# Performance work log

Hardware: AMD Instinct MI355X
Metric: run time of the kernel (lower is better)

## Reference

```python
import jax, jax.numpy as jnp
import numpy as np
from jax import lax

T, B, N_IN, H, N_OUT = 2048, 64, 128, 256, 128

def setup_inputs() -> dict:
    key = jax.random.key(0)
    ks = jax.random.split(key, 7)
    s_ih = 1.0 / np.sqrt(H)
    return {
        "x": jax.random.normal(ks[0], (T, B, N_IN), jnp.float32),
        "w_ih": jax.random.uniform(ks[1], (H, N_IN), jnp.float32, -s_ih, s_ih),
        "w_hh": jax.random.uniform(ks[2], (H, H), jnp.float32, -s_ih, s_ih),
        "b_ih": jax.random.uniform(ks[3], (H,), jnp.float32, -s_ih, s_ih),
        "b_hh": jax.random.uniform(ks[4], (H,), jnp.float32, -s_ih, s_ih),
        "w_out": jax.random.uniform(ks[5], (N_OUT, H), jnp.float32, -1.0/np.sqrt(H), 1.0/np.sqrt(H)),
        "b_out": jax.random.uniform(ks[6], (N_OUT,), jnp.float32, -1.0/np.sqrt(H), 1.0/np.sqrt(H)),
    }

def reference(x, w_ih, w_hh, b_ih, b_hh, w_out, b_out):
    # Vanilla RNN (basic_rnn_step): h_t = tanh(x_t W_ih^T + b_ih + h_{t-1} W_hh^T + b_hh)
    # Precompute input projections for all timesteps in one big GEMM.
    x_proj = jnp.einsum('tbi,hi->tbh', x, w_ih) + b_ih + b_hh  # [T,B,H]

    def step(h, xp_t):
        h = jnp.tanh(xp_t + h @ w_hh.T)
        return h, h

    h0 = jnp.zeros((x.shape[1], w_hh.shape[0]), x.dtype)
    _, hs = lax.scan(step, h0, x_proj)          # hs: [T,B,H]
    # Linear output layer applied at every timestep (has_fc_out -> logits)
    return jnp.einsum('tbh,oh->tbo', hs, w_out) + b_out
```

## Files before the change

### kernel.cpp

```cpp
#include <hip/hip_runtime.h>
#include <hip/hip_bf16.h>
#include <hip/hip_fp16.h>

#define T_ 2048
#define B_ 64
#define NIN_ 128
#define H_ 256
#define NOUT_ 128
#define TB_ (T_*B_)
#define BH_ (B_*H_)
#define TBLK2_ (T_/16)

typedef _Float16 h8 __attribute__((ext_vector_type(8)));
typedef float f32x4 __attribute__((ext_vector_type(4)));

#define BAR_LGKM() asm volatile("s_waitcnt lgkmcnt(0)\n\ts_barrier" ::: "memory")

__device__ __forceinline__ h8 cvt8(float4 a, float4 b) {
    h8 r;
    r[0] = (_Float16)a.x; r[1] = (_Float16)a.y; r[2] = (_Float16)a.z; r[3] = (_Float16)a.w;
    r[4] = (_Float16)b.x; r[5] = (_Float16)b.y; r[6] = (_Float16)b.z; r[7] = (_Float16)b.w;
    return r;
}
__device__ __forceinline__ h8 ld_cvt8(const float* __restrict__ p) {
    const float4* q = (const float4*)p;
    return cvt8(q[0], q[1]);
}

__global__ __launch_bounds__(768, 1) void k2_scan(
    const float* __restrict__ x,
    const float* __restrict__ w_ih,
    const float* __restrict__ w_hh,
    const float* __restrict__ b_ih,
    const float* __restrict__ b_hh,
    _Float16* __restrict__ hs)
{
    const int tid = threadIdx.x;
    const int lane = tid & 63, wave = tid >> 6;
    const int n = lane & 15, quad = lane >> 4;
    const int b = blockIdx.x;

    __shared__ __align__(16) _Float16 hb[2][256];
    __shared__ __align__(16) _Float16 xpb[2][256][24];

    if (wave < 8) {
        const int tsel = quad & 1;
        const int j = wave*32 + tsel*16 + n;
        const bool writer = (quad < 2);

        h8 bf[2][8];
        #pragma unroll
        for (int t = 0; t < 2; ++t)
            #pragma unroll
            for (int kt = 0; kt < 8; ++kt)
                bf[t][kt] = ld_cvt8(w_hh + (size_t)(wave*32 + t*16 + n) * H_ + kt*32 + quad*8);

        if (tid < 256) hb[0][tid] = (_Float16)0.0f;
        asm volatile("s_waitcnt lgkmcnt(0) vmcnt(0)" ::: "memory");
        __builtin_amdgcn_s_barrier();

        _Float16* hsl = hs + (size_t)b * H_ + j;

#define K2_STEP(T, RB, WB, XV)                                                 \
    {                                                                          \
        const h8* hp = (const h8*)&RB[0];                                      \
        h8 av[8];                                                              \
        _Pragma("unroll")                                                      \
        for (int kt = 0; kt < 8; ++kt) av[kt] = hp[kt*4 + quad];               \
        f32x4 acc[2];                                                          \
        acc[0] = (f32x4){0,0,0,0}; acc[1] = (f32x4){0,0,0,0};                  \
        __builtin_amdgcn_s_setprio(1);                                         \
        _Pragma("unroll")                                                      \
        for (int kt = 0; kt < 8; ++kt) {                                       \
            acc[0] = __builtin_amdgcn_mfma_f32_16x16x32_f16(av[kt], bf[0][kt], acc[0], 0, 0, 0); \
            acc[1] = __builtin_amdgcn_mfma_f32_16x16x32_f16(av[kt], bf[1][kt], acc[1], 0, 0, 0); \
        }                                                                      \
        __builtin_amdgcn_s_setprio(0);                                         \
        float vv = tsel ? acc[1][0] : acc[0][0];                               \
        float sv = vv + (XV);                                                  \
        float e  = __expf(2.0f * sv);                                          \
        float hn = fmaf(-2.0f, __builtin_amdgcn_rcpf(e + 1.0f), 1.0f);         \
        _Float16 h16 = (_Float16)hn;                                           \
        if (writer) {                                                          \
            WB[j] = h16;                                                       \
            hsl[(size_t)(T) * BH_] = h16;                                      \
        }                                                                      \
        BAR_LGKM();                                                            \
    }

        for (int tb = 0; tb < TBLK2_; ++tb) {
            const int p = tb & 1;
            const int t0 = tb * 16;
            h8 cur0 = *(const h8*)&xpb[p][j][0];
            K2_STEP(t0 + 0, hb[0], hb[1], (float)cur0[0])
            K2_STEP(t0 + 1, hb[1], hb[0], (float)cur0[1])
            K2_STEP(t0 + 2, hb[0], hb[1], (float)cur0[2])
            K2_STEP(t0 + 3, hb[1], hb[0], (float)cur0[3])
            K2_STEP(t0 + 4, hb[0], hb[1], (float)cur0[4])
            K2_STEP(t0 + 5, hb[1], hb[0], (float)cur0[5])
            K2_STEP(t0 + 6, hb[0], hb[1], (float)cur0[6])
            K2_STEP(t0 + 7, hb[1], hb[0], (float)cur0[7])
            h8 cur1 = *(const h8*)&xpb[p][j][8];
            K2_STEP(t0 + 8,  hb[0], hb[1], (float)cur1[0])
            K2_STEP(t0 + 9,  hb[1], hb[0], (float)cur1[1])
            K2_STEP(t0 + 10, hb[0], hb[1], (float)cur1[2])
            K2_STEP(t0 + 11, hb[1], hb[0], (float)cur1[3])
            K2_STEP(t0 + 12, hb[0], hb[1], (float)cur1[4])
            K2_STEP(t0 + 13, hb[1], hb[0], (float)cur1[5])
            K2_STEP(t0 + 14, hb[0], hb[1], (float)cur1[6])
            K2_STEP(t0 + 15, hb[1], hb[0], (float)cur1[7])
        }
#undef K2_STEP
    } else {
        const int w = wave - 8;
        const int m = n;

        h8 aih[4][4];
        #pragma unroll
        for (int i = 0; i < 4; ++i)
            #pragma unroll
            for (int kt = 0; kt < 4; ++kt)
                aih[i][kt] = ld_cvt8(w_ih + (size_t)(w*64 + i*16 + m) * NIN_ + kt*32 + quad*8);

        float xb2[4][4];
        #pragma unroll
        for (int i = 0; i < 4; ++i)
            #pragma unroll
            for (int r = 0; r < 4; ++r) {
                int c = w*64 + i*16 + quad*4 + r;
                xb2[i][r] = b_ih[c] + b_hh[c];
            }

        float4 xr[4][2];
        h8 bx[4];
        f32x4 xacc[4];

#define LOAD_X(blk)                                                            \
    {                                                                          \
        _Pragma("unroll")                                                      \
        for (int kt = 0; kt < 4; ++kt) {                                       \
            const float4* q = (const float4*)(x + ((size_t)((blk)*16 + m) * B_ + b) * NIN_ + kt*32 + quad*8); \
            xr[kt][0] = q[0]; xr[kt][1] = q[1];                                \
        }                                                                      \
    }

#define XPROJ_PIECE(kt)                                                        \
    {                                                                          \
        _Pragma("unroll")                                                      \
        for (int i = 0; i < 4; ++i)                                            \
            xacc[i] = __builtin_amdgcn_mfma_f32_16x16x32_f16(aih[i][kt], bx[kt], xacc[i], 0, 0, 0); \
    }

#define XPROJ_WRITE(buf)                                                       \
    {                                                                          \
        _Pragma("unroll")                                                      \
        for (int i = 0; i < 4; ++i)                                            \
            _Pragma("unroll")                                                  \
            for (int r = 0; r < 4; ++r) {                                      \
                int c = w*64 + i*16 + quad*4 + r;                              \
                xpb[buf][c][m] = (_Float16)(xacc[i][r] + xb2[i][r]);           \
            }                                                                  \
    }

        LOAD_X(0);
        #pragma unroll
        for (int kt = 0; kt < 4; ++kt) bx[kt] = cvt8(xr[kt][0], xr[kt][1]);
        #pragma unroll
        for (int i = 0; i < 4; ++i) xacc[i] = (f32x4){0,0,0,0};
        #pragma unroll
        for (int kt = 0; kt < 4; ++kt) XPROJ_PIECE(kt)
        XPROJ_WRITE(0);
        LOAD_X(1);
        asm volatile("s_waitcnt lgkmcnt(0) vmcnt(0)" ::: "memory");
        __builtin_amdgcn_s_barrier();

        for (int tb = 0; tb < TBLK2_; ++tb) {
            const int p = tb & 1;
            const bool gen = (tb < TBLK2_ - 1);
            if (gen) {
                #pragma unroll
                for (int kt = 0; kt < 4; ++kt) bx[kt] = cvt8(xr[kt][0], xr[kt][1]);
                #pragma unroll
                for (int i = 0; i < 4; ++i) xacc[i] = (f32x4){0,0,0,0};
            }
            __builtin_amdgcn_sched_barrier(0);
            BAR_LGKM();
            if (gen) { XPROJ_PIECE(0) }
            __builtin_amdgcn_sched_barrier(0);
            BAR_LGKM();
            if (gen) { XPROJ_PIECE(1) }
            __builtin_amdgcn_sched_barrier(0);
            BAR_LGKM();
            if (gen) { XPROJ_PIECE(2) }
            __builtin_amdgcn_sched_barrier(0);
            BAR_LGKM();
            if (gen) { XPROJ_PIECE(3) }
            __builtin_amdgcn_sched_barrier(0);
            BAR_LGKM();
            BAR_LGKM();
            if (gen) { XPROJ_WRITE(p ^ 1); }
            BAR_LGKM();
            if (tb < TBLK2_ - 2) { LOAD_X(tb + 2); }
            BAR_LGKM();
            BAR_LGKM();
            BAR_LGKM();
            BAR_LGKM();
            BAR_LGKM();
            BAR_LGKM();
            BAR_LGKM();
            BAR_LGKM();
            BAR_LGKM();
        }
#undef LOAD_X
#undef XPROJ_PIECE
#undef XPROJ_WRITE
    }
}

__global__ __launch_bounds__(256, 1) void k3_out(
    const _Float16* __restrict__ hs,
    const float* __restrict__ w_out,
    const float* __restrict__ b_out,
    float* __restrict__ out)
{
    const int tid = threadIdx.x;
    const int lane = tid & 63, wave = tid >> 6;
    const int m = lane & 15, quad = lane >> 4;

    h8 af[8][8];
    #pragma unroll
    for (int i = 0; i < 8; ++i)
        #pragma unroll
        for (int kt = 0; kt < 8; ++kt)
            af[i][kt] = ld_cvt8(w_out + (size_t)(i*16 + m) * H_ + kt*32 + quad*8);

    __shared__ __align__(16) float st[4][16][132];

    const size_t base = (size_t)blockIdx.x * 512 + (size_t)wave * 16;

    h8 nxt[8];
    #pragma unroll
    for (int kt = 0; kt < 8; ++kt)
        nxt[kt] = *(const h8*)(hs + (base + m) * H_ + kt*32 + quad*8);

    for (int it = 0; it < 8; ++it) {
        const size_t n0 = base + (size_t)it * 64;

        h8 cur[8];
        #pragma unroll
        for (int kt = 0; kt < 8; ++kt) cur[kt] = nxt[kt];

        if (it < 7) {
            #pragma unroll
            for (int kt = 0; kt < 8; ++kt)
                nxt[kt] = *(const h8*)(hs + (n0 + 64 + m) * H_ + kt*32 + quad*8);
        }

        f32x4 acc[8];
        #pragma unroll
        for (int i = 0; i < 8; ++i) acc[i] = (f32x4){0,0,0,0};
        #pragma unroll
        for (int kt = 0; kt < 8; ++kt)
            #pragma unroll
            for (int i = 0; i < 8; ++i)
                acc[i] = __builtin_amdgcn_mfma_f32_16x16x32_f16(af[i][kt], cur[kt], acc[i], 0, 0, 0);

        #pragma unroll
        for (int i = 0; i < 8; ++i)
            *(f32x4*)&st[wave][m][i*16 + quad*4] = acc[i];
        asm volatile("s_waitcnt lgkmcnt(0)" ::: "memory");

        #pragma unroll
        for (int c = 0; c < 8; ++c) {
            int idx = lane + c*64;
            int r = idx >> 5, c4 = (idx & 31) * 4;
            f32x4 v = *(const f32x4*)&st[wave][r][c4];
            f32x4 bb = *(const f32x4*)(b_out + c4);
            v[0] += bb[0]; v[1] += bb[1]; v[2] += bb[2]; v[3] += bb[3];
            *(f32x4*)(out + (n0 + r) * NOUT_ + c4) = v;
        }
    }
}

extern "C" void kernel_launch(void* const* d_in, const int* in_sizes, int n_in,
                              void* d_out, int out_size, void* d_ws, size_t ws_size,
                              hipStream_t stream) {
    const float* x     = (const float*)d_in[0];
    const float* w_ih  = (const float*)d_in[1];
    const float* w_hh  = (const float*)d_in[2];
    const float* b_ih  = (const float*)d_in[3];
    const float* b_hh  = (const float*)d_in[4];
    const float* w_out = (const float*)d_in[5];
    const float* b_out = (const float*)d_in[6];

    _Float16* hsbuf = (_Float16*)d_ws;

    k2_scan<<<B_,  768, 0, stream>>>(x, w_ih, w_hh, b_ih, b_hh, hsbuf);
    k3_out <<<256, 256, 0, stream>>>(hsbuf, w_out, b_out, (float*)d_out);
}
```

Baseline: 860.0 us.

## Fuse output projection into the recurrent scan kernel via LDS history buffer

Adds four output waves to the scan block. They read each 16-step chunk of hidden states from a double-buffered LDS history, run the W_out GEMM with MFMA one chunk behind the recurrence, and write the logits directly. This removes the fp16 hidden-state round trip through global memory and the second kernel launch. In exchange it adds waves that share every lockstep barrier, along with extra LDS traffic and scattered global stores that could slow the latency-critical serial scan.

```diff
diff --git a/kernel.cpp b/kernel.cpp
--- a/kernel.cpp
+++ b/kernel.cpp
@@ -27,13 +27,15 @@
     return cvt8(q[0], q[1]);
 }
 
-__global__ __launch_bounds__(768, 1) void k2_scan(
+__global__ __launch_bounds__(1024, 1) void k2_fused(
     const float* __restrict__ x,
     const float* __restrict__ w_ih,
     const float* __restrict__ w_hh,
     const float* __restrict__ b_ih,
     const float* __restrict__ b_hh,
-    _Float16* __restrict__ hs)
+    const float* __restrict__ w_out,
+    const float* __restrict__ b_out,
+    float* __restrict__ out)
 {
     const int tid = threadIdx.x;
     const int lane = tid & 63, wave = tid >> 6;
@@ -42,6 +44,7 @@
 
     __shared__ __align__(16) _Float16 hb[2][256];
     __shared__ __align__(16) _Float16 xpb[2][256][24];
+    __shared__ __align__(16) _Float16 hist[2][16][264];
 
     if (wave < 8) {
         const int tsel = quad & 1;
@@ -59,9 +62,7 @@
         asm volatile("s_waitcnt lgkmcnt(0) vmcnt(0)" ::: "memory");
         __builtin_amdgcn_s_barrier();
 
-        _Float16* hsl = hs + (size_t)b * H_ + j;
-
-#define K2_STEP(T, RB, WB, XV)                                                 \
+#define K2_STEP(C, RB, WB, XV)                                                 \
     {                                                                          \
         const h8* hp = (const h8*)&RB[0];                                      \
         h8 av[8];                                                              \
@@ -83,35 +84,34 @@
         _Float16 h16 = (_Float16)hn;                                           \
         if (writer) {                                                          \
             WB[j] = h16;                                                       \
-            hsl[(size_t)(T) * BH_] = h16;                                      \
+            hist[p][C][j] = h16;                                               \
         }                                                                      \
         BAR_LGKM();                                                            \
     }
 
         for (int tb = 0; tb < TBLK2_; ++tb) {
             const int p = tb & 1;
-            const int t0 = tb * 16;
             h8 cur0 = *(const h8*)&xpb[p][j][0];
-            K2_STEP(t0 + 0, hb[0], hb[1], (float)cur0[0])
-            K2_STEP(t0 + 1, hb[1], hb[0], (float)cur0[1])
-            K2_STEP(t0 + 2, hb[0], hb[1], (float)cur0[2])
-            K2_STEP(t0 + 3, hb[1], hb[0], (float)cur0[3])
-            K2_STEP(t0 + 4, hb[0], hb[1], (float)cur0[4])
-            K2_STEP(t0 + 5, hb[1], hb[0], (float)cur0[5])
-            K2_STEP(t0 + 6, hb[0], hb[1], (float)cur0[6])
-            K2_STEP(t0 + 7, hb[1], hb[0], (float)cur0[7])
+            K2_STEP(0,  hb[0], hb[1], (float)cur0[0])
+            K2_STEP(1,  hb[1], hb[0], (float)cur0[1])
+            K2_STEP(2,  hb[0], hb[1], (float)cur0[2])
+            K2_STEP(3,  hb[1], hb[0], (float)cur0[3])
+            K2_STEP(4,  hb[0], hb[1], (float)cur0[4])
+            K2_STEP(5,  hb[1], hb[0], (float)cur0[5])
+            K2_STEP(6,  hb[0], hb[1], (float)cur0[6])
+            K2_STEP(7,  hb[1], hb[0], (float)cur0[7])
             h8 cur1 = *(const h8*)&xpb[p][j][8];
-            K2_STEP(t0 + 8,  hb[0], hb[1], (float)cur1[0])
-            K2_STEP(t0 + 9,  hb[1], hb[0], (float)cur1[1])
-            K2_STEP(t0 + 10, hb[0], hb[1], (float)cur1[2])
-            K2_STEP(t0 + 11, hb[1], hb[0], (float)cur1[3])
-            K2_STEP(t0 + 12, hb[0], hb[1], (float)cur1[4])
-            K2_STEP(t0 + 13, hb[1], hb[0], (float)cur1[5])
-            K2_STEP(t0 + 14, hb[0], hb[1], (float)cur1[6])
-            K2_STEP(t0 + 15, hb[1], hb[0], (float)cur1[7])
+            K2_STEP(8,  hb[0], hb[1], (float)cur1[0])
+            K2_STEP(9,  hb[1], hb[0], (float)cur1[1])
+            K2_STEP(10, hb[0], hb[1], (float)cur1[2])
+            K2_STEP(11, hb[1], hb[0], (float)cur1[3])
+            K2_STEP(12, hb[0], hb[1], (float)cur1[4])
+            K2_STEP(13, hb[1], hb[0], (float)cur1[5])
+            K2_STEP(14, hb[0], hb[1], (float)cur1[6])
+            K2_STEP(15, hb[1], hb[0], (float)cur1[7])
         }
 #undef K2_STEP
-    } else {
+    } else if (wave < 12) {
         const int w = wave - 8;
         const int m = n;
 
@@ -214,71 +214,90 @@
 #undef LOAD_X
 #undef XPROJ_PIECE
 #undef XPROJ_WRITE
-    }
-}
-
-__global__ __launch_bounds__(256, 1) void k3_out(
-    const _Float16* __restrict__ hs,
-    const float* __restrict__ w_out,
-    const float* __restrict__ b_out,
-    float* __restrict__ out)
-{
-    const int tid = threadIdx.x;
-    const int lane = tid & 63, wave = tid >> 6;
-    const int m = lane & 15, quad = lane >> 4;
-
-    h8 af[8][8];
-    #pragma unroll
-    for (int i = 0; i < 8; ++i)
-        #pragma unroll
-        for (int kt = 0; kt < 8; ++kt)
-            af[i][kt] = ld_cvt8(w_out + (size_t)(i*16 + m) * H_ + kt*32 + quad*8);
-
-    __shared__ __align__(16) float st[4][16][132];
-
-    const size_t base = (size_t)blockIdx.x * 512 + (size_t)wave * 16;
-
-    h8 nxt[8];
-    #pragma unroll
-    for (int kt = 0; kt < 8; ++kt)
-        nxt[kt] = *(const h8*)(hs + (base + m) * H_ + kt*32 + quad*8);
-
-    for (int it = 0; it < 8; ++it) {
-        const size_t n0 = base + (size_t)it * 64;
-
-        h8 cur[8];
-        #pragma unroll
-        for (int kt = 0; kt < 8; ++kt) cur[kt] = nxt[kt];
-
-        if (it < 7) {
+    } else {
+        const int ow = wave - 12;
+        const int wcol = ow * 32;
+
+        h8 bo[2][8];
+        #pragma unroll
+        for (int t2 = 0; t2 < 2; ++t2)
             #pragma unroll
             for (int kt = 0; kt < 8; ++kt)
-                nxt[kt] = *(const h8*)(hs + (n0 + 64 + m) * H_ + kt*32 + quad*8);
+                bo[t2][kt] = ld_cvt8(w_out + (size_t)(wcol + t2*16 + n) * H_ + kt*32 + quad*8);
+
+        float ob[2];
+        #pragma unroll
+        for (int t2 = 0; t2 < 2; ++t2) ob[t2] = b_out[wcol + t2*16 + n];
+
+        asm volatile("s_waitcnt lgkmcnt(0) vmcnt(0)" ::: "memory");
+        __builtin_amdgcn_s_barrier();
+
+#define XO_PIECE(kt)                                                           \
+    {                                                                          \
+        oacc[0] = __builtin_amdgcn_mfma_f32_16x16x32_f16(av2[kt], bo[0][kt], oacc[0], 0, 0, 0); \
+        oacc[1] = __builtin_amdgcn_mfma_f32_16x16x32_f16(av2[kt], bo[1][kt], oacc[1], 0, 0, 0); \
+    }
+#define XO_STORE(TP0)                                                          \
+    {                                                                          \
+        _Pragma("unroll")                                                      \
+        for (int t2 = 0; t2 < 2; ++t2)                                         \
+            _Pragma("unroll")                                                  \
+            for (int r = 0; r < 4; ++r)                                        \
+                out[((size_t)((TP0) + quad*4 + r) * B_ + b) * NOUT_ + wcol + t2*16 + n] = oacc[t2][r] + ob[t2]; \
+    }
+
+        for (int tb = 0; tb < TBLK2_; ++tb) {
+            const int pp = (tb & 1) ^ 1;
+            const bool run = (tb > 0);
+            h8 av2[8];
+            f32x4 oacc[2];
+            if (run) {
+                #pragma unroll
+                for (int kt = 0; kt < 8; ++kt)
+                    av2[kt] = *(const h8*)&hist[pp][n][kt*32 + quad*8];
+                oacc[0] = (f32x4){0,0,0,0}; oacc[1] = (f32x4){0,0,0,0};
+            }
+            __builtin_amdgcn_sched_barrier(0);
+            BAR_LGKM();
+            if (run) { XO_PIECE(0) XO_PIECE(1) }
+            __builtin_amdgcn_sched_barrier(0);
+            BAR_LGKM();
+            if (run) { XO_PIECE(2) XO_PIECE(3) }
+            __builtin_amdgcn_sched_barrier(0);
+            BAR_LGKM();
+            if (run) { XO_PIECE(4) XO_PIECE(5) }
+            __builtin_amdgcn_sched_barrier(0);
+            BAR_LGKM();
+            if (run) { XO_PIECE(6) XO_PIECE(7) }
+            __builtin_amdgcn_sched_barrier(0);
+            BAR_LGKM();
+            BAR_LGKM();
+            if (run) { XO_STORE((tb - 1) * 16) }
+            BAR_LGKM();
+            BAR_LGKM();
+            BAR_LGKM();
+            BAR_LGKM();
+            BAR_LGKM();
+            BAR_LGKM();
+            BAR_LGKM();
+            BAR_LGKM();
+            BAR_LGKM();
+            BAR_LGKM();
         }
-
-        f32x4 acc[8];
-        #pragma unroll
-        for (int i = 0; i < 8; ++i) acc[i] = (f32x4){0,0,0,0};
-        #pragma unroll
-        for (int kt = 0; kt < 8; ++kt)
-            #pragma unroll
-            for (int i = 0; i < 8; ++i)
-                acc[i] = __builtin_amdgcn_mfma_f32_16x16x32_f16(af[i][kt], cur[kt], acc[i], 0, 0, 0);
-
-        #pragma unroll
-        for (int i = 0; i < 8; ++i)
-            *(f32x4*)&st[wave][m][i*16 + quad*4] = acc[i];
-        asm volatile("s_waitcnt lgkmcnt(0)" ::: "memory");
-
-        #pragma unroll
-        for (int c = 0; c < 8; ++c) {
-            int idx = lane + c*64;
-            int r = idx >> 5, c4 = (idx & 31) * 4;
-            f32x4 v = *(const f32x4*)&st[wave][r][c4];
-            f32x4 bb = *(const f32x4*)(b_out + c4);
-            v[0] += bb[0]; v[1] += bb[1]; v[2] += bb[2]; v[3] += bb[3];
-            *(f32x4*)(out + (n0 + r) * NOUT_ + c4) = v;
+        {
+            const int pp = (TBLK2_ - 1) & 1;
+            h8 av2[8];
+            #pragma unroll
+            for (int kt = 0; kt < 8; ++kt)
+                av2[kt] = *(const h8*)&hist[pp][n][kt*32 + quad*8];
+            f32x4 oacc[2];
+            oacc[0] = (f32x4){0,0,0,0}; oacc[1] = (f32x4){0,0,0,0};
+            #pragma unroll
+            for (int kt = 0; kt < 8; ++kt) XO_PIECE(kt)
+            XO_STORE((TBLK2_ - 1) * 16)
         }
+#undef XO_PIECE
+#undef XO_STORE
     }
 }
 
@@ -293,8 +312,6 @@
     const float* w_out = (const float*)d_in[5];
     const float* b_out = (const float*)d_in[6];
 
-    _Float16* hsbuf = (_Float16*)d_ws;
-
-    k2_scan<<<B_,  768, 0, stream>>>(x, w_ih, w_hh, b_ih, b_hh, hsbuf);
-    k3_out <<<256, 256, 0, stream>>>(hsbuf, w_out, b_out, (float*)d_out);
+    k2_fused<<<B_, 1024, 0, stream>>>(x, w_ih, w_hh, b_ih, b_hh,
+                                      w_out, b_out, (float*)d_out);
 }
```

Measured after the change: 844.1 us. About the same (-1.8%).
